# Performance work log

Hardware: AMD Instinct MI355X
Metric: run time of the kernel (lower is better)

The kernel has to match this reference:

```python
import jax, jax.numpy as jnp
import numpy as np

NEG_INF = -1e30


def _cc_attention(q, k, v):
    # q,k: [B,H,W,c], v: [B,H,W,C]
    B, H, W, _ = q.shape
    # vertical scores over column: [B,H,W,H], diag (h==g) masked out
    sv = jnp.einsum('bhwc,bgwc->bhwg', q, k)
    eye = jnp.eye(H, dtype=bool)[:, None, :]  # [H,1,H]
    sv = jnp.where(eye, NEG_INF, sv)
    # horizontal scores over row: [B,H,W,W]
    sh = jnp.einsum('bhwc,bhuc->bhwu', q, k)
    a = jax.nn.softmax(jnp.concatenate([sv, sh], axis=-1), axis=-1)
    av, ah = a[..., :H], a[..., H:H + W]
    yv = jnp.einsum('bhwg,bgwc->bhwc', av, v)
    yh = jnp.einsum('bhwu,bhuc->bhwc', ah, v)
    return yv + yh


def setup_inputs() -> dict:
    key = jax.random.key(0)
    ks = jax.random.split(key, 7)
    B, H, W, C = 8, 96, 96, 512
    c = C // 8
    s = lambda n: 1.0 / np.sqrt(n)
    return {
        'x': jax.random.normal(ks[0], (B, H, W, C), jnp.float32),
        'Wq': jax.random.normal(ks[1], (C, c), jnp.float32) * s(C),
        'bq': jnp.zeros((c,), jnp.float32),
        'Wk': jax.random.normal(ks[2], (C, c), jnp.float32) * s(C),
        'bk': jnp.zeros((c,), jnp.float32),
        'Wv': jax.random.normal(ks[3], (C, C), jnp.float32) * s(C),
        'bv': jnp.zeros((C,), jnp.float32),
        'gamma': jnp.float32(0.5),
    }


def reference(x, Wq, bq, Wk, bk, Wv, bv, gamma):
    # 1x1 convs == per-pixel matmul
    q = jnp.einsum('bhwc,cd->bhwd', x, Wq) + bq
    k = jnp.einsum('bhwc,cd->bhwd', x, Wk) + bk
    v = jnp.einsum('bhwc,cd->bhwd', x, Wv) + bv
    y = _cc_attention(q, k, v) * gamma
    return y + x
```

## Files before the change

kernel.cpp:

```cpp
#include <hip/hip_runtime.h>
#include <hip/hip_bf16.h>


#define NPIX 73728
#define CC 512
#define CQ 64
#define PA 384

typedef __attribute__((ext_vector_type(8))) short bf16x8;
typedef __attribute__((ext_vector_type(4))) float f32x4;

__device__ __forceinline__ short bf16s(float f) {
    __hip_bfloat16 h = __float2bfloat16(f);
    return *reinterpret_cast<short*>(&h);
}

__device__ __forceinline__ float bf2f(short s) {
    return __uint_as_float(((unsigned int)(unsigned short)s) << 16);
}

__global__ __launch_bounds__(256) void conv_w3(
    const float* __restrict__ Wq, const float* __restrict__ Wk,
    const float* __restrict__ Wv,
    short* __restrict__ Wqf, short* __restrict__ Wkf, short* __restrict__ Wvf)
{
    int bid = blockIdx.x;
    const float* W; short* dst; int J; int base;
    if (bid < 16)      { W = Wq; dst = Wqf; J = 64;  base = 0;  }
    else if (bid < 32) { W = Wk; dst = Wkf; J = 64;  base = 16; }
    else               { W = Wv; dst = Wvf; J = 512; base = 32; }
    int idx = (bid - base) * 256 + threadIdx.x;
    int lane = idx & 63;
    int blk = idx >> 6;
    int ntiles = J >> 4;
    int ntile = blk % ntiles;
    int kb32 = blk / ntiles;
    int krow = kb32 * 32 + (lane >> 4) * 8;
    int col = ntile * 16 + (lane & 15);
    union { short h[8]; uint4 u; } pk;
    #pragma unroll
    for (int j = 0; j < 8; ++j)
        pk.h[j] = bf16s(W[(size_t)(krow + j) * J + col]);
    *reinterpret_cast<uint4*>(dst + (size_t)idx * 8) = pk.u;
}

__global__ __launch_bounds__(256) void proj_qk(
    const float* __restrict__ x,
    const short* __restrict__ Wqf, const short* __restrict__ Wkf,
    const float* __restrict__ bq, const float* __restrict__ bk,
    short* __restrict__ q, short* __restrict__ k)
{
    __shared__ __align__(16) short Sbuf[128 * 136];
    const int tid = threadIdx.x;
    const int lane = tid & 63;
    const int w = tid >> 6;
    const int mBase = blockIdx.x * 128;
    const int wr = w >> 1;
    const int wsel = w & 1;
    const short* Wf = wsel ? Wkf : Wqf;
    const float* bias = wsel ? bk : bq;

    f32x4 acc[4][4];
    #pragma unroll
    for (int i = 0; i < 4; ++i)
        #pragma unroll
        for (int j = 0; j < 4; ++j) {
            f32x4 z = {0.f, 0.f, 0.f, 0.f};
            acc[i][j] = z;
        }

    for (int kb = 0; kb < 16; ++kb) {
        #pragma unroll
        for (int s = 0; s < 2; ++s) {
            int G = tid + 256 * s;
            int dl = G & 63;
            int row = ((G >> 6) << 4) + (dl & 15);
            const float* src = x + (size_t)(mBase + row) * 512 + kb * 32 + (dl >> 4) * 8;
            float4 f0 = *reinterpret_cast<const float4*>(src);
            float4 f1 = *reinterpret_cast<const float4*>(src + 4);
            union { short h[8]; bf16x8 v; } pk;
            pk.h[0] = bf16s(f0.x); pk.h[1] = bf16s(f0.y);
            pk.h[2] = bf16s(f0.z); pk.h[3] = bf16s(f0.w);
            pk.h[4] = bf16s(f1.x); pk.h[5] = bf16s(f1.y);
            pk.h[6] = bf16s(f1.z); pk.h[7] = bf16s(f1.w);
            *reinterpret_cast<bf16x8*>(&Sbuf[G * 8]) = pk.v;
        }
        __syncthreads();

        bf16x8 bf[4], af[4];
        #pragma unroll
        for (int jn = 0; jn < 4; ++jn)
            bf[jn] = *reinterpret_cast<const bf16x8*>(
                Wf + ((size_t)(kb * 4 + jn) * 64 + lane) * 8);
        #pragma unroll
        for (int i = 0; i < 4; ++i)
            af[i] = *reinterpret_cast<const bf16x8*>(&Sbuf[(wr * 4 + i) * 512 + lane * 8]);
        #pragma unroll
        for (int i = 0; i < 4; ++i)
            #pragma unroll
            for (int jn = 0; jn < 4; ++jn)
                acc[i][jn] = __builtin_amdgcn_mfma_f32_16x16x32_bf16(
                    af[i], bf[jn], acc[i][jn], 0, 0, 0);
        __syncthreads();
    }

    const int lrow = (lane >> 4) * 4, cl = lane & 15;
    #pragma unroll
    for (int jn = 0; jn < 4; ++jn) {
        float bc = bias[jn * 16 + cl];
        #pragma unroll
        for (int i = 0; i < 4; ++i) {
            int row = wr * 64 + i * 16 + lrow;
            #pragma unroll
            for (int r = 0; r < 4; ++r)
                Sbuf[(row + r) * 136 + wsel * 64 + jn * 16 + cl] =
                    bf16s(acc[i][jn][r] + bc);
        }
    }
    __syncthreads();
    #pragma unroll
    for (int i = 0; i < 8; ++i) {
        int id = tid + 256 * i;
        int arr = id >> 10;
        int rem = id & 1023;
        int pix = rem >> 3, cc = rem & 7;
        bf16x8 vv = *reinterpret_cast<const bf16x8*>(&Sbuf[pix * 136 + arr * 64 + cc * 8]);
        short* dst = arr ? k : q;
        *reinterpret_cast<bf16x8*>(dst + (size_t)(mBase + pix) * 64 + cc * 8) = vv;
    }
}

__global__ __launch_bounds__(256) void proj_v(
    const float* __restrict__ x, const short* __restrict__ Wvf,
    const float* __restrict__ bv, short* __restrict__ vth)
{
    __shared__ __align__(16) short Albuf[128 * 32];
    const int tid = threadIdx.x;
    const int lane = tid & 63;
    const int w = tid >> 6;
    const int bid = blockIdx.x;
    const int xcd = bid & 7;
    const int jj = bid >> 3;
    const int slab = jj & 3;
    const int g = (jj >> 2) * 8 + xcd;
    const int mBase = g * 128;
    const int nBase = slab * 128;

    const int wr = w >> 1, wc = w & 1;
    const int nTile0 = (nBase >> 4) + wc * 4;

    f32x4 acc[4][4];
    #pragma unroll
    for (int i = 0; i < 4; ++i)
        #pragma unroll
        for (int j = 0; j < 4; ++j) {
            f32x4 z = {0.f, 0.f, 0.f, 0.f};
            acc[i][j] = z;
        }

    for (int kb = 0; kb < 16; ++kb) {
        #pragma unroll
        for (int s = 0; s < 2; ++s) {
            int G = tid + 256 * s;
            int dl = G & 63;
            int row = ((G >> 6) << 4) + (dl & 15);
            const float* src = x + (size_t)(mBase + row) * 512 + kb * 32 + (dl >> 4) * 8;
            float4 f0 = *reinterpret_cast<const float4*>(src);
            float4 f1 = *reinterpret_cast<const float4*>(src + 4);
            union { short h[8]; bf16x8 v; } pk;
            pk.h[0] = bf16s(f0.x); pk.h[1] = bf16s(f0.y);
            pk.h[2] = bf16s(f0.z); pk.h[3] = bf16s(f0.w);
            pk.h[4] = bf16s(f1.x); pk.h[5] = bf16s(f1.y);
            pk.h[6] = bf16s(f1.z); pk.h[7] = bf16s(f1.w);
            *reinterpret_cast<bf16x8*>(&Albuf[G * 8]) = pk.v;
        }
        __syncthreads();

        bf16x8 bf[4], af[4];
        #pragma unroll
        for (int jn = 0; jn < 4; ++jn)
            bf[jn] = *reinterpret_cast<const bf16x8*>(
                Wvf + ((size_t)(kb * 32 + nTile0 + jn) * 64 + lane) * 8);
        #pragma unroll
        for (int i = 0; i < 4; ++i)
            af[i] = *reinterpret_cast<const bf16x8*>(&Albuf[(wr * 4 + i) * 512 + lane * 8]);
        #pragma unroll
        for (int i = 0; i < 4; ++i)
            #pragma unroll
            for (int jn = 0; jn < 4; ++jn)
                acc[i][jn] = __builtin_amdgcn_mfma_f32_16x16x32_bf16(
                    af[i], bf[jn], acc[i][jn], 0, 0, 0);
        __syncthreads();
    }

    const int lrow = (lane >> 4) * 4, lcol = lane & 15;
    #pragma unroll
    for (int jn = 0; jn < 4; ++jn) {
        int col = nBase + wc * 64 + jn * 16 + lcol;
        float bc = bv[col];
        #pragma unroll
        for (int i = 0; i < 4; ++i) {
            int row = mBase + wr * 64 + i * 16 + lrow;
            short4 st;
            st.x = bf16s(acc[i][jn][0] + bc);
            st.y = bf16s(acc[i][jn][1] + bc);
            st.z = bf16s(acc[i][jn][2] + bc);
            st.w = bf16s(acc[i][jn][3] + bc);
            *reinterpret_cast<short4*>(vth + (size_t)col * NPIX + row) = st;
        }
    }
}

__global__ __launch_bounds__(256) void transpose_vtv(
    const short* __restrict__ vth, short* __restrict__ vtv)
{
    __shared__ short T[96 * 97];
    const int tid = threadIdx.x;
    const size_t plane = (size_t)blockIdx.x * 9216;
    const short* src = vth + plane;
    short* dst = vtv + plane;

    for (int id = tid; id < 1152; id += 256) {
        int h = id / 12, w8 = (id % 12) * 8;
        bf16x8 v = *reinterpret_cast<const bf16x8*>(src + h * 96 + w8);
        #pragma unroll
        for (int j = 0; j < 8; ++j) T[h * 97 + w8 + j] = v[j];
    }
    __syncthreads();
    for (int id = tid; id < 1152; id += 256) {
        int ww = id / 12, h8 = (id % 12) * 8;
        union { short h[8]; bf16x8 v; } pk;
        #pragma unroll
        for (int j = 0; j < 8; ++j) pk.h[j] = T[(h8 + j) * 97 + ww];
        *reinterpret_cast<bf16x8*>(dst + ww * 96 + h8) = pk.v;
    }
}

__global__ __launch_bounds__(256) void cc_scores(
    const short* __restrict__ Q,
    const short* __restrict__ K,
    float* __restrict__ S)
{
    __shared__ __align__(16) float Ss[96 * 100];
    const int tid = threadIdx.x;
    const int lane = tid & 63;
    const int wv = tid >> 6;
    const int wr = wv >> 1, wc = wv & 1;
    const bool vert = (blockIdx.y == 0);
    const int b = blockIdx.x / 96;
    const int line = blockIdx.x % 96;

    size_t base;
    int rowStride;
    if (vert) { base = (size_t)b * 9216 + line;       rowStride = 96; }
    else      { base = ((size_t)b * 96 + line) * 96;  rowStride = 1;  }

    const int cl = lane & 15;
    const int q8 = (lane >> 4) * 8;

    f32x4 acc[3][3];
    #pragma unroll
    for (int i = 0; i < 3; ++i)
        #pragma unroll
        for (int j = 0; j < 3; ++j) {
            f32x4 z = {0.f, 0.f, 0.f, 0.f};
            acc[i][j] = z;
        }

    #pragma unroll
    for (int kb = 0; kb < 2; ++kb) {
        bf16x8 af[3], bf[3];
        #pragma unroll
        for (int mt = 0; mt < 3; ++mt) {
            size_t n = base + (size_t)(wr * 48 + mt * 16 + cl) * rowStride;
            af[mt] = *reinterpret_cast<const bf16x8*>(Q + n * 64 + kb * 32 + q8);
        }
        #pragma unroll
        for (int nt = 0; nt < 3; ++nt) {
            size_t n = base + (size_t)(wc * 48 + nt * 16 + cl) * rowStride;
            bf[nt] = *reinterpret_cast<const bf16x8*>(K + n * 64 + kb * 32 + q8);
        }
        #pragma unroll
        for (int mt = 0; mt < 3; ++mt)
            #pragma unroll
            for (int nt = 0; nt < 3; ++nt)
                acc[mt][nt] = __builtin_amdgcn_mfma_f32_16x16x32_bf16(
                    af[mt], bf[nt], acc[mt][nt], 0, 0, 0);
    }

    const int lrow = (lane >> 4) * 4;
    #pragma unroll
    for (int mt = 0; mt < 3; ++mt) {
        #pragma unroll
        for (int r = 0; r < 4; ++r) {
            int i = wr * 48 + mt * 16 + lrow + r;
            #pragma unroll
            for (int nt = 0; nt < 3; ++nt) {
                int j = wc * 48 + nt * 16 + cl;
                Ss[i * 100 + j] = (vert && i == j) ? -1e30f : acc[mt][nt][r];
            }
        }
    }
    __syncthreads();

    const int dirOff = vert ? 0 : 96;
    #pragma unroll
    for (int t = 0; t < 9; ++t) {
        int id = tid + 256 * t;
        int i = id / 24, j4 = (id % 24) * 4;
        f32x4 v = *reinterpret_cast<const f32x4*>(&Ss[i * 100 + j4]);
        size_t n = base + (size_t)i * rowStride;
        *reinterpret_cast<f32x4*>(S + n * 192 + dirOff + j4) = v;
    }
}

__global__ __launch_bounds__(256) void cc_softmax(float* __restrict__ S)
{
    const int tid = threadIdx.x;
    const int lane = tid & 63;
    const size_t n = (size_t)blockIdx.x * 4 + (tid >> 6);
    float* row = S + n * 192;
    float s0 = row[lane], s1 = row[lane + 64], s2 = row[lane + 128];
    float m = fmaxf(s0, fmaxf(s1, s2));
    #pragma unroll
    for (int off = 32; off >= 1; off >>= 1) m = fmaxf(m, __shfl_xor(m, off, 64));
    float e0 = expf(s0 - m), e1 = expf(s1 - m), e2 = expf(s2 - m);
    float sum = e0 + e1 + e2;
    #pragma unroll
    for (int off = 32; off >= 1; off >>= 1) sum += __shfl_xor(sum, off, 64);
    float inv = 1.0f / sum;
    short p0 = bf16s(e0 * inv);
    short p1 = bf16s(e1 * inv);
    short p2 = bf16s(e2 * inv);
    short* av = reinterpret_cast<short*>(row);
    short* ah = av + 96;
    av[lane] = p0;
    if (lane < 32) av[64 + lane] = p1;
    else           ah[lane - 32] = p1;
    ah[32 + lane] = p2;
}

__global__ __launch_bounds__(256) void cc_aggr_v(
    const short* __restrict__ A,
    const short* __restrict__ vtv,
    short* __restrict__ Yv)
{
    __shared__ __align__(16) short Yb[96 * 136];
    const int tid = threadIdx.x;
    const int lane = tid & 63;
    const int wv = tid >> 6;
    const int bid = blockIdx.x;
    const int pair = bid >> 2;
    const int cBase = (bid & 3) * 128;
    const int b = pair / 96;
    const int w = pair - b * 96;
    const size_t pixBase = (size_t)b * 9216 + w;
    const size_t wBase = (size_t)b * 9216 + (size_t)w * 96;

    const int wr = wv >> 1, wc = wv & 1;
    const int cl = lane & 15, q = lane >> 4;

    f32x4 acc[3][4];
    #pragma unroll
    for (int i = 0; i < 3; ++i)
        #pragma unroll
        for (int j = 0; j < 4; ++j) {
            f32x4 z = {0.f, 0.f, 0.f, 0.f};
            acc[i][j] = z;
        }

    #pragma unroll
    for (int kb = 0; kb < 3; ++kb) {
        bf16x8 af[3];
        #pragma unroll
        for (int mt = 0; mt < 3; ++mt) {
            size_t n = pixBase + (size_t)(wr * 48 + mt * 16 + cl) * 96;
            af[mt] = *reinterpret_cast<const bf16x8*>(A + n * PA + kb * 32 + q * 8);
        }
        #pragma unroll
        for (int nt = 0; nt < 4; ++nt) {
            int col = cBase + wc * 64 + nt * 16 + cl;
            bf16x8 bv = *reinterpret_cast<const bf16x8*>(
                vtv + (size_t)col * NPIX + wBase + kb * 32 + q * 8);
            #pragma unroll
            for (int mt = 0; mt < 3; ++mt)
                acc[mt][nt] = __builtin_amdgcn_mfma_f32_16x16x32_bf16(
                    af[mt], bv, acc[mt][nt], 0, 0, 0);
        }
    }

    const int lrow = q * 4;
    #pragma unroll
    for (int mt = 0; mt < 3; ++mt) {
        #pragma unroll
        for (int r = 0; r < 4; ++r) {
            int hl = wr * 48 + mt * 16 + lrow + r;
            #pragma unroll
            for (int nt = 0; nt < 4; ++nt)
                Yb[hl * 136 + wc * 64 + nt * 16 + cl] = bf16s(acc[mt][nt][r]);
        }
    }
    __syncthreads();
    #pragma unroll
    for (int i = 0; i < 6; ++i) {
        int id = tid + 256 * i;
        int hh = id >> 4, cc = id & 15;
        bf16x8 v = *reinterpret_cast<const bf16x8*>(&Yb[hh * 136 + cc * 8]);
        *reinterpret_cast<bf16x8*>(
            Yv + (pixBase + (size_t)hh * 96) * 512 + cBase + cc * 8) = v;
    }
}

__global__ __launch_bounds__(256) void cc_aggr_h_final(
    const short* __restrict__ A,
    const short* __restrict__ vth,
    const short* __restrict__ Yv,
    const float* __restrict__ X,
    const float* __restrict__ gamma_p,
    float* __restrict__ out)
{
    __shared__ __align__(16) float Yh[96 * 132];
    const int tid = threadIdx.x;
    const int lane = tid & 63;
    const int wv = tid >> 6;
    const int bid = blockIdx.x;
    const int pair = bid >> 2;
    const int cBase = (bid & 3) * 128;
    const size_t rowBase = (size_t)pair * 96;

    const int wr = wv >> 1, wc = wv & 1;
    const int cl = lane & 15, q = lane >> 4;

    f32x4 acc[3][4];
    #pragma unroll
    for (int i = 0; i < 3; ++i)
        #pragma unroll
        for (int j = 0; j < 4; ++j) {
            f32x4 z = {0.f, 0.f, 0.f, 0.f};
            acc[i][j] = z;
        }

    #pragma unroll
    for (int kb = 0; kb < 3; ++kb) {
        bf16x8 af[3];
        #pragma unroll
        for (int mt = 0; mt < 3; ++mt) {
            size_t n = rowBase + (size_t)(wr * 48 + mt * 16 + cl);
            af[mt] = *reinterpret_cast<const bf16x8*>(A + n * PA + 96 + kb * 32 + q * 8);
        }
        #pragma unroll
        for (int nt = 0; nt < 4; ++nt) {
            int col = cBase + wc * 64 + nt * 16 + cl;
            bf16x8 bv = *reinterpret_cast<const bf16x8*>(
                vth + (size_t)col * NPIX + rowBase + kb * 32 + q * 8);
            #pragma unroll
            for (int mt = 0; mt < 3; ++mt)
                acc[mt][nt] = __builtin_amdgcn_mfma_f32_16x16x32_bf16(
                    af[mt], bv, acc[mt][nt], 0, 0, 0);
        }
    }

    const int lrow = q * 4;
    #pragma unroll
    for (int mt = 0; mt < 3; ++mt) {
        #pragma unroll
        for (int r = 0; r < 4; ++r) {
            int wl = wr * 48 + mt * 16 + lrow + r;
            #pragma unroll
            for (int nt = 0; nt < 4; ++nt)
                Yh[wl * 132 + wc * 64 + nt * 16 + cl] = acc[mt][nt][r];
        }
    }
    __syncthreads();

    const float gm = gamma_p[0];
    #pragma unroll
    for (int i = 0; i < 12; ++i) {
        int id = tid + 256 * i;
        int rw = id >> 5, c4 = (id & 31) * 4;
        f32x4 yh = *reinterpret_cast<const f32x4*>(&Yh[rw * 132 + c4]);
        size_t off = (rowBase + rw) * 512 + cBase + c4;
        float4 xx = *reinterpret_cast<const float4*>(X + off);
        short4 yv = *reinterpret_cast<const short4*>(Yv + off);
        float4 o;
        o.x = (yh[0] + bf2f(yv.x)) * gm + xx.x;
        o.y = (yh[1] + bf2f(yv.y)) * gm + xx.y;
        o.z = (yh[2] + bf2f(yv.z)) * gm + xx.z;
        o.w = (yh[3] + bf2f(yv.w)) * gm + xx.w;
        *reinterpret_cast<float4*>(out + off) = o;
    }
}

extern "C" void kernel_launch(void* const* d_in, const int* in_sizes, int n_in,
                              void* d_out, int out_size, void* d_ws, size_t ws_size,
                              hipStream_t stream) {
    const float* x     = (const float*)d_in[0];
    const float* Wq    = (const float*)d_in[1];
    const float* bq    = (const float*)d_in[2];
    const float* Wk    = (const float*)d_in[3];
    const float* bk    = (const float*)d_in[4];
    const float* Wv    = (const float*)d_in[5];
    const float* bv    = (const float*)d_in[6];
    const float* gamma = (const float*)d_in[7];
    float* out = (float*)d_out;

    short* Wqf = (short*)d_ws;
    short* Wkf = Wqf + 512 * 64;
    short* Wvf = Wkf + 512 * 64;
    short* q   = Wvf + 512 * 512;
    short* k   = q + (size_t)NPIX * CQ;
    short* vth = k + (size_t)NPIX * CQ;
    short* vtv = vth + (size_t)NPIX * CC;
    short* Yv  = vtv + (size_t)NPIX * CC;
    float* S   = (float*)(Yv + (size_t)NPIX * CC);

    conv_w3<<<160, 256, 0, stream>>>(Wq, Wk, Wv, Wqf, Wkf, Wvf);

    proj_qk<<<NPIX / 128, 256, 0, stream>>>(x, Wqf, Wkf, bq, bk, q, k);
    proj_v<<<(NPIX / 128) * 4, 256, 0, stream>>>(x, Wvf, bv, vth);
    transpose_vtv<<<4096, 256, 0, stream>>>(vth, vtv);

    cc_scores<<<dim3(8 * 96, 2), 256, 0, stream>>>(q, k, S);
    cc_softmax<<<NPIX / 4, 256, 0, stream>>>(S);

    cc_aggr_v<<<768 * 4, 256, 0, stream>>>((const short*)S, vtv, Yv);
    cc_aggr_h_final<<<768 * 4, 256, 0, stream>>>(
        (const short*)S, vth, Yv, x, gamma, out);
}
```

Before: 584.8 us.

## Load projection A-fragments directly from global into registers with prefetch

In proj_qk and proj_v, the A operand (x converted to bf16) is no longer staged through shared memory with barriers. Each wave loads its own fp32 rows straight into registers in MFMA fragment layout and converts them there. The next k-step's A and B fragments are prefetched while the current MFMAs run. This removes LDS traffic and two __syncthreads per iteration, but waves sharing rows now load and convert x redundantly and register pressure rises.

```diff
diff --git a/kernel.cpp b/kernel.cpp
--- a/kernel.cpp
+++ b/kernel.cpp
@@ -17,6 +17,15 @@
 
 __device__ __forceinline__ float bf2f(short s) {
     return __uint_as_float(((unsigned int)(unsigned short)s) << 16);
+}
+
+__device__ __forceinline__ bf16x8 pack8(float4 f0, float4 f1) {
+    union { short h[8]; bf16x8 v; } pk;
+    pk.h[0] = bf16s(f0.x); pk.h[1] = bf16s(f0.y);
+    pk.h[2] = bf16s(f0.z); pk.h[3] = bf16s(f0.w);
+    pk.h[4] = bf16s(f1.x); pk.h[5] = bf16s(f1.y);
+    pk.h[6] = bf16s(f1.z); pk.h[7] = bf16s(f1.w);
+    return pk.v;
 }
 
 __global__ __launch_bounds__(256) void conv_w3(
@@ -60,6 +69,9 @@
     const short* Wf = wsel ? Wkf : Wqf;
     const float* bias = wsel ? bk : bq;
 
+    const float* aBase = x + (size_t)(mBase + wr * 64 + (lane & 15)) * 512
+                           + (lane >> 4) * 8;
+
     f32x4 acc[4][4];
     #pragma unroll
     for (int i = 0; i < 4; ++i)
@@ -69,39 +81,42 @@
             acc[i][j] = z;
         }
 
+    float4 pa[4][2];
+    bf16x8 pb[4];
+    #pragma unroll
+    for (int i = 0; i < 4; ++i) {
+        const float* p = aBase + (size_t)i * 16 * 512;
+        pa[i][0] = *reinterpret_cast<const float4*>(p);
+        pa[i][1] = *reinterpret_cast<const float4*>(p + 4);
+    }
+    #pragma unroll
+    for (int jn = 0; jn < 4; ++jn)
+        pb[jn] = *reinterpret_cast<const bf16x8*>(Wf + ((size_t)jn * 64 + lane) * 8);
+
     for (int kb = 0; kb < 16; ++kb) {
-        #pragma unroll
-        for (int s = 0; s < 2; ++s) {
-            int G = tid + 256 * s;
-            int dl = G & 63;
-            int row = ((G >> 6) << 4) + (dl & 15);
-            const float* src = x + (size_t)(mBase + row) * 512 + kb * 32 + (dl >> 4) * 8;
-            float4 f0 = *reinterpret_cast<const float4*>(src);
-            float4 f1 = *reinterpret_cast<const float4*>(src + 4);
-            union { short h[8]; bf16x8 v; } pk;
-            pk.h[0] = bf16s(f0.x); pk.h[1] = bf16s(f0.y);
-            pk.h[2] = bf16s(f0.z); pk.h[3] = bf16s(f0.w);
-            pk.h[4] = bf16s(f1.x); pk.h[5] = bf16s(f1.y);
-            pk.h[6] = bf16s(f1.z); pk.h[7] = bf16s(f1.w);
-            *reinterpret_cast<bf16x8*>(&Sbuf[G * 8]) = pk.v;
-        }
-        __syncthreads();
-
-        bf16x8 bf[4], af[4];
-        #pragma unroll
-        for (int jn = 0; jn < 4; ++jn)
-            bf[jn] = *reinterpret_cast<const bf16x8*>(
-                Wf + ((size_t)(kb * 4 + jn) * 64 + lane) * 8);
-        #pragma unroll
-        for (int i = 0; i < 4; ++i)
-            af[i] = *reinterpret_cast<const bf16x8*>(&Sbuf[(wr * 4 + i) * 512 + lane * 8]);
+        bf16x8 af[4], bf[4];
+        #pragma unroll
+        for (int i = 0; i < 4; ++i) af[i] = pack8(pa[i][0], pa[i][1]);
+        #pragma unroll
+        for (int jn = 0; jn < 4; ++jn) bf[jn] = pb[jn];
+        if (kb < 15) {
+            #pragma unroll
+            for (int i = 0; i < 4; ++i) {
+                const float* p = aBase + (size_t)i * 16 * 512 + (kb + 1) * 32;
+                pa[i][0] = *reinterpret_cast<const float4*>(p);
+                pa[i][1] = *reinterpret_cast<const float4*>(p + 4);
+            }
+            #pragma unroll
+            for (int jn = 0; jn < 4; ++jn)
+                pb[jn] = *reinterpret_cast<const bf16x8*>(
+                    Wf + ((size_t)((kb + 1) * 4 + jn) * 64 + lane) * 8);
+        }
         #pragma unroll
         for (int i = 0; i < 4; ++i)
             #pragma unroll
             for (int jn = 0; jn < 4; ++jn)
                 acc[i][jn] = __builtin_amdgcn_mfma_f32_16x16x32_bf16(
                     af[i], bf[jn], acc[i][jn], 0, 0, 0);
-        __syncthreads();
     }
 
     const int lrow = (lane >> 4) * 4, cl = lane & 15;
@@ -134,7 +149,6 @@
     const float* __restrict__ x, const short* __restrict__ Wvf,
     const float* __restrict__ bv, short* __restrict__ vth)
 {
-    __shared__ __align__(16) short Albuf[128 * 32];
     const int tid = threadIdx.x;
     const int lane = tid & 63;
     const int w = tid >> 6;
@@ -149,6 +163,9 @@
     const int wr = w >> 1, wc = w & 1;
     const int nTile0 = (nBase >> 4) + wc * 4;
 
+    const float* aBase = x + (size_t)(mBase + wr * 64 + (lane & 15)) * 512
+                           + (lane >> 4) * 8;
+
     f32x4 acc[4][4];
     #pragma unroll
     for (int i = 0; i < 4; ++i)
@@ -158,39 +175,43 @@
             acc[i][j] = z;
         }
 
+    float4 pa[4][2];
+    bf16x8 pb[4];
+    #pragma unroll
+    for (int i = 0; i < 4; ++i) {
+        const float* p = aBase + (size_t)i * 16 * 512;
+        pa[i][0] = *reinterpret_cast<const float4*>(p);
+        pa[i][1] = *reinterpret_cast<const float4*>(p + 4);
+    }
+    #pragma unroll
+    for (int jn = 0; jn < 4; ++jn)
+        pb[jn] = *reinterpret_cast<const bf16x8*>(
+            Wvf + ((size_t)(nTile0 + jn) * 64 + lane) * 8);
+
     for (int kb = 0; kb < 16; ++kb) {
-        #pragma unroll
-        for (int s = 0; s < 2; ++s) {
-            int G = tid + 256 * s;
-            int dl = G & 63;
-            int row = ((G >> 6) << 4) + (dl & 15);
-            const float* src = x + (size_t)(mBase + row) * 512 + kb * 32 + (dl >> 4) * 8;
-            float4 f0 = *reinterpret_cast<const float4*>(src);
-            float4 f1 = *reinterpret_cast<const float4*>(src + 4);
-            union { short h[8]; bf16x8 v; } pk;
-            pk.h[0] = bf16s(f0.x); pk.h[1] = bf16s(f0.y);
-            pk.h[2] = bf16s(f0.z); pk.h[3] = bf16s(f0.w);
-            pk.h[4] = bf16s(f1.x); pk.h[5] = bf16s(f1.y);
-            pk.h[6] = bf16s(f1.z); pk.h[7] = bf16s(f1.w);
-            *reinterpret_cast<bf16x8*>(&Albuf[G * 8]) = pk.v;
-        }
-        __syncthreads();
-
-        bf16x8 bf[4], af[4];
-        #pragma unroll
-        for (int jn = 0; jn < 4; ++jn)
-            bf[jn] = *reinterpret_cast<const bf16x8*>(
-                Wvf + ((size_t)(kb * 32 + nTile0 + jn) * 64 + lane) * 8);
-        #pragma unroll
-        for (int i = 0; i < 4; ++i)
-            af[i] = *reinterpret_cast<const bf16x8*>(&Albuf[(wr * 4 + i) * 512 + lane * 8]);
+        bf16x8 af[4], bf[4];
+        #pragma unroll
+        for (int i = 0; i < 4; ++i) af[i] = pack8(pa[i][0], pa[i][1]);
+        #pragma unroll
+        for (int jn = 0; jn < 4; ++jn) bf[jn] = pb[jn];
+        if (kb < 15) {
+            #pragma unroll
+            for (int i = 0; i < 4; ++i) {
+                const float* p = aBase + (size_t)i * 16 * 512 + (kb + 1) * 32;
+                pa[i][0] = *reinterpret_cast<const float4*>(p);
+                pa[i][1] = *reinterpret_cast<const float4*>(p + 4);
+            }
+            #pragma unroll
+            for (int jn = 0; jn < 4; ++jn)
+                pb[jn] = *reinterpret_cast<const bf16x8*>(
+                    Wvf + ((size_t)((kb + 1) * 32 + nTile0 + jn) * 64 + lane) * 8);
+        }
         #pragma unroll
         for (int i = 0; i < 4; ++i)
             #pragma unroll
             for (int jn = 0; jn < 4; ++jn)
                 acc[i][jn] = __builtin_amdgcn_mfma_f32_16x16x32_bf16(
                     af[i], bf[jn], acc[i][jn], 0, 0, 0);
-        __syncthreads();
     }
 
     const int lrow = (lane >> 4) * 4, lcol = lane & 15;
```

New measurement: 640.9 us. 1.1x slower.
